# Kernel tuning notes

Hardware: AMD Instinct MI355X
Metric: run time of the kernel (lower is better)

The kernel has to match this reference:

```python
import jax, jax.numpy as jnp
import numpy as np

NH = 4
TEMP = 0.5

def _ln(x, w, b):
    mu = x.mean(-1, keepdims=True)
    var = ((x - mu) ** 2).mean(-1, keepdims=True)
    return (x - mu) / jnp.sqrt(var + 1e-5) * w + b

def _encoder(x, bias, key_pad, layers):
    # pre-LN torch TransformerEncoder, relu FFN, dropout=0
    Wqkv, bqkv, Wo, bo, ln1w, ln1b, ln2w, ln2b, W1, b1, W2, b2 = layers
    B, L, H = x.shape
    d = H // NH
    scale = 1.0 / np.sqrt(d)
    for i in range(Wqkv.shape[0]):
        y = _ln(x, ln1w[i], ln1b[i])
        qkv = y @ Wqkv[i].T + bqkv[i]
        q, k, v = jnp.split(qkv, 3, axis=-1)
        q = q.reshape(B, L, NH, d).transpose(0, 2, 1, 3)
        k = k.reshape(B, L, NH, d).transpose(0, 2, 1, 3)
        v = v.reshape(B, L, NH, d).transpose(0, 2, 1, 3)
        s = jnp.einsum('bhqd,bhkd->bhqk', q, k) * scale
        if bias is not None:
            s = s + bias
        s = s + key_pad[:, None, None, :]
        a = jax.nn.softmax(s, axis=-1)
        o = jnp.einsum('bhqk,bhkd->bhqd', a, v).transpose(0, 2, 1, 3).reshape(B, L, H)
        x = x + o @ Wo[i].T + bo[i]
        y = _ln(x, ln2w[i], ln2b[i])
        x = x + jax.nn.relu(y @ W1[i].T + b1[i]) @ W2[i].T + b2[i]
    return x

def _layer_params(key, nl, H, F, sc=0.05):
    ks = jax.random.split(key, 4)
    return (jax.random.normal(ks[0], (nl, 3 * H, H)) * sc, jnp.zeros((nl, 3 * H)),
            jax.random.normal(ks[1], (nl, H, H)) * sc, jnp.zeros((nl, H)),
            jnp.ones((nl, H)), jnp.zeros((nl, H)), jnp.ones((nl, H)), jnp.zeros((nl, H)),
            jax.random.normal(ks[2], (nl, F, H)) * sc, jnp.zeros((nl, F)),
            jax.random.normal(ks[3], (nl, H, F)) * sc, jnp.zeros((nl, H)))

def setup_inputs():
    key = jax.random.key(0)
    IN, H, ED, F = 64, 128, 16, 256
    G, NPG = 8, 512
    N = G * NPG
    m, k = 4, 16
    T = N
    S = T * m
    EPS = 24
    E_loc = S * EPS
    E = 65536
    ks = jax.random.split(key, 13)
    x = jax.random.normal(ks[0], (N, IN))
    log_probs = -jnp.abs(jax.random.normal(ks[1], (S,)))
    root = jnp.repeat(jnp.arange(T), m)
    base = (root // NPG) * NPG
    rest = base[:, None] + jax.random.randint(ks[2], (S, k - 1), 0, NPG)
    nodes_sampled = jnp.concatenate([root[:, None], rest], axis=1)
    valid = jnp.ones((S * k,), dtype=bool)
    edge_index_sampled = jax.random.randint(ks[3], (2, E_loc), 0, k)
    edge_ptr = jnp.arange(S + 1) * EPS
    ea_flat = jax.random.normal(ks[4], (E_loc, ED))
    src = jax.random.randint(ks[5], (E,), 0, N)
    dst = (src // NPG) * NPG + jax.random.randint(ks[6], (E,), 0, NPG)
    edge_index = jnp.stack([src, dst])
    edge_attr = jax.random.normal(ks[7], (E, ED))
    batch_vec = jnp.arange(N) // NPG
    ptr = jnp.arange(G + 1) * NPG
    d = dict(x=x, log_probs=log_probs, ea_flat=ea_flat, edge_attr=edge_attr,
             init_W=jax.random.normal(ks[8], (H, IN + 2)) * 0.05, init_b=jnp.zeros((H,)),
             loc_ep_W=jax.random.normal(ks[9], (NH, ED)) * 0.05, loc_ep_b=jnp.zeros((NH,)),
             glob_ep_W=jax.random.normal(ks[10], (NH, ED)) * 0.05, glob_ep_b=jnp.zeros((NH,)),
             loc_nw=jnp.ones((H,)), loc_nb=jnp.zeros((H,)),
             glob_nw=jnp.ones((H,)), glob_nb=jnp.zeros((H,)),
             nodes_sampled=nodes_sampled, edge_index_sampled=edge_index_sampled,
             edge_ptr=edge_ptr, edge_index=edge_index, batch_vec=batch_vec,
             ptr=ptr, valid=valid)
    names = ['Wqkv', 'bqkv', 'Wo', 'bo', 'ln1w', 'ln1b', 'ln2w', 'ln2b', 'W1', 'b1', 'W2', 'b2']
    for n, a in zip(names, _layer_params(ks[11], 4, H, F)):
        d['loc_' + n] = a
    for n, a in zip(names, _layer_params(ks[12], 4, H, F)):
        d['glob_' + n] = a
    return d

def reference(x, log_probs, ea_flat, edge_attr, init_W, init_b, loc_ep_W, loc_ep_b,
              glob_ep_W, glob_ep_b, loc_nw, loc_nb, glob_nw, glob_nb,
              loc_Wqkv, loc_bqkv, loc_Wo, loc_bo, loc_ln1w, loc_ln1b, loc_ln2w, loc_ln2b,
              loc_W1, loc_b1, loc_W2, loc_b2,
              glob_Wqkv, glob_bqkv, glob_Wo, glob_bo, glob_ln1w, glob_ln1b, glob_ln2w, glob_ln2b,
              glob_W1, glob_b1, glob_W2, glob_b2,
              nodes_sampled, edge_index_sampled, edge_ptr, edge_index, batch_vec, ptr, valid):
    S, k = nodes_sampled.shape
    N = x.shape[0]
    T = N
    m = S // T
    G = ptr.shape[0] - 1
    max_N = N // G  # equal-size graphs
    H = init_W.shape[0]
    # ---- phase 1: flatten subgraphs + init features ----
    x_flat = x[nodes_sampled.reshape(-1)]                         # [S*k, IN]
    root_global = jnp.repeat(jnp.arange(T), m)                    # [S]
    root_local = jnp.argmax(nodes_sampled == root_global[:, None], axis=1)
    root_mask = jnp.zeros((S * k,), x.dtype).at[jnp.arange(S) * k + root_local].set(1.0)
    lp = jnp.where(jnp.isfinite(log_probs), log_probs, 0.0)
    lp_flat = jnp.repeat(lp, k)[:, None] * valid[:, None].astype(x.dtype)
    h = jnp.concatenate([x_flat, lp_flat, root_mask[:, None]], axis=1) @ init_W.T + init_b
    # ---- local edge bias (scatter-add) ----
    E_loc = ea_flat.shape[0]
    sub = jnp.searchsorted(edge_ptr, jnp.arange(E_loc), side='right') - 1
    eap = ea_flat @ loc_ep_W.T + loc_ep_b                         # [E_loc, NH]
    lbias = jnp.zeros((S, k, k, NH), x.dtype).at[sub, edge_index_sampled[0], edge_index_sampled[1]].add(eap).transpose(0, 3, 1, 2)
    v2 = valid.reshape(S, k)
    key_pad_l = jnp.where(v2, 0.0, -1e9).astype(x.dtype)
    loc_layers = (loc_Wqkv, loc_bqkv, loc_Wo, loc_bo, loc_ln1w, loc_ln1b, loc_ln2w, loc_ln2b, loc_W1, loc_b1, loc_W2, loc_b2)
    out = _encoder(h.reshape(S, k, H), lbias, key_pad_l, loc_layers)
    out = _ln(out, loc_nw, loc_nb)
    vf = v2.astype(x.dtype)[..., None]
    sub_embs = (out * vf).sum(1) / jnp.maximum(vf.sum(1), 1.0)    # [S, H]
    # ---- weighted-mean aggregation over m samples per target node ----
    w = jax.nn.softmax(log_probs.reshape(T, m) / TEMP, axis=1)
    node_embs = jnp.einsum('tm,tmh->th', w, sub_embs.reshape(T, m, H))
    # ---- global phase: to_dense_batch + edge-bias transformer ----
    pos = jnp.arange(N) - ptr[batch_vec]
    dense = jnp.zeros((G, max_N, H), x.dtype).at[batch_vec, pos].set(node_embs)
    vmask = jnp.zeros((G, max_N), bool).at[batch_vec, pos].set(True)
    g = batch_vec[edge_index[0]]
    sl = edge_index[0] - ptr[g]
    dl = edge_index[1] - ptr[g]
    eag = edge_attr @ glob_ep_W.T + glob_ep_b
    gbias = jnp.zeros((G, max_N, max_N, NH), x.dtype).at[g, sl, dl].add(eag).transpose(0, 3, 1, 2)
    key_pad_g = jnp.where(vmask, 0.0, -1e9).astype(x.dtype)
    glob_layers = (glob_Wqkv, glob_bqkv, glob_Wo, glob_bo, glob_ln1w, glob_ln1b, glob_ln2w, glob_ln2b, glob_W1, glob_b1, glob_W2, glob_b2)
    gout = _encoder(dense, gbias, key_pad_g, glob_layers)
    gout = _ln(gout, glob_nw, glob_nb)
    return (gout * vmask[..., None].astype(x.dtype)).sum(1)      # [G, H]
```

## Files before the change

### kernel.cpp

```cpp
#include <hip/hip_runtime.h>
#include <math.h>

#define IN_F      64
#define H_DIM     128
#define NH_       4
#define DH_       32
#define FF_DIM    256
#define KSUB      16
#define S_SEQ     16384
#define E_LOC     393216
#define G_NUM     8
#define NPG_      512
#define N_NODES   4096
#define E_GLOB    65536
#define NLAYERS   4
#define SCALE_ATT 0.17677669529663687f

#define WQKV_SZ   (3*H_DIM*H_DIM)
#define WO_SZ     (H_DIM*H_DIM)
#define W1_SZ     (FF_DIM*H_DIM)
#define W2_SZ     (H_DIM*FF_DIM)

#define ATT(sg)   (4352 + (sg) * 2560)
#define PS_OFF    9472
// ... 350 lines not shown
            for (int sg = 0; sg < 2; ++sg)
                #pragma unroll
                for (int kt = 0; kt < 4; ++kt)
                    ao[sg][kt] = *(const bf16x8*)(stg + sg * 2176 + r * 136 + kt * 32 + q * 8);
            const unsigned short* wr0 = wo_l + (size_t)r * H_DIM + q * 8;
            bf16x8 co[4], no[4];
            #pragma unroll
            for (int kt = 0; kt < 4; ++kt) co[kt] = *(const bf16x8*)(wr0 + kt * 32);
            for (int nt = 0; nt < 8; ++nt) {
                if (nt < 7) {
                    const unsigned short* wn = wr0 + (size_t)(nt + 1) * 2048;
                    #pragma unroll
                    for (int kt = 0; kt < 4; ++kt) no[kt] = *(const bf16x8*)(wn + kt * 32);
                }
                f32x4 aA = {0.f,0.f,0.f,0.f}, aB = {0.f,0.f,0.f,0.f};
                PRIO_HI();
                #pragma unroll
                for (int kt = 0; kt < 4; ++kt) {
                    aA = mfma16(ao[0][kt], co[kt], aA);
                    aB = mfma16(ao[1][kt], co[kt], aB);
                }
                PRIO_LO();
                float bov = bo[l * H_DIM + nt * 16 + r];
                #pragma unroll
                for (int i = 0; i < 4; ++i) {
                    X[0][nt][i] += aA[i] + bov;
                    X[1][nt][i] += aB[i] + bov;
                }
                #pragma unroll
                for (int kt = 0; kt < 4; ++kt) co[kt] = no[kt];
            }
        }

        ln_to_row(X[0], ln2w + l * H_DIM, ln2b + l * H_DIM, stg, r, q);
        ln_to_row(X[1], ln2w + l * H_DIM, ln2b + l * H_DIM, stg + 2176, r, q);

        {
            bf16x8 a2[2][4];
            #pragma unroll
            for (int sg = 0; sg < 2; ++sg)
                #pragma unroll
                for (int kt = 0; kt < 4; ++kt)
                    a2[sg][kt] = *(const bf16x8*)(stg + sg * 2176 + r * 136 + kt * 32 + q * 8);
            const unsigned short* wr0 = w1_l + (size_t)r * H_DIM + q * 8;
            bf16x8 c1b[4], n1b[4];
            #pragma unroll
            for (int kt = 0; kt < 4; ++kt) c1b[kt] = *(const bf16x8*)(wr0 + kt * 32);
            for (int nt = 0; nt < 16; ++nt) {
                if (nt < 15) {
                    const unsigned short* wn = wr0 + (size_t)(nt + 1) * 2048;
                    #pragma unroll
                    for (int kt = 0; kt < 4; ++kt) n1b[kt] = *(const bf16x8*)(wn + kt * 32);
                }
                float b1v = b1[l * FF_DIM + nt * 16 + r];
                #pragma unroll
                for (int sg = 0; sg < 2; ++sg) {
                    f32x4 acc = {0.f,0.f,0.f,0.f};
                    PRIO_HI();
                    #pragma unroll
                    for (int kt = 0; kt < 4; ++kt) acc = mfma16(a2[sg][kt], c1b[kt], acc);
                    PRIO_LO();
                    float f0 = fmaxf(acc[0] + b1v, 0.f), f1 = fmaxf(acc[1] + b1v, 0.f);
                    float f2 = fmaxf(acc[2] + b1v, 0.f), f3 = fmaxf(acc[3] + b1v, 0.f);
                    unsigned flo = cvt_pk(f0, f1), fhi = cvt_pk(f2, f3);
                    stg[sg * 4224 + (q * 4 + 0) * 264 + nt * 16 + r] = (unsigned short)flo;
                    stg[sg * 4224 + (q * 4 + 1) * 264 + nt * 16 + r] = (unsigned short)(flo >> 16);
                    stg[sg * 4224 + (q * 4 + 2) * 264 + nt * 16 + r] = (unsigned short)fhi;
                    stg[sg * 4224 + (q * 4 + 3) * 264 + nt * 16 + r] = (unsigned short)(fhi >> 16);
                }
                #pragma unroll
                for (int kt = 0; kt < 4; ++kt) c1b[kt] = n1b[kt];
            }
            for (int kp = 0; kp < 2; ++kp) {
                bf16x8 a1[2][4];
                #pragma unroll
                for (int sg = 0; sg < 2; ++sg)
                    #pragma unroll
                    for (int kt = 0; kt < 4; ++kt)
                        a1[sg][kt] = *(const bf16x8*)(stg + sg * 4224 + r * 264 + kp * 128 + kt * 32 + q * 8);
                const unsigned short* wr2 = w2_l + (size_t)r * FF_DIM + kp * 128 + q * 8;
                bf16x8 c2b[4], n2b[4];
                #pragma unroll
                for (int kt = 0; kt < 4; ++kt) c2b[kt] = *(const bf16x8*)(wr2 + kt * 32);
                for (int nt = 0; nt < 8; ++nt) {
                    if (nt < 7) {
                        const unsigned short* wn = wr2 + (size_t)(nt + 1) * 4096;
                        #pragma unroll
                        for (int kt = 0; kt < 4; ++kt) n2b[kt] = *(const bf16x8*)(wn + kt * 32);
                    }
                    f32x4 aA = {0.f,0.f,0.f,0.f}, aB = {0.f,0.f,0.f,0.f};
                    PRIO_HI();
                    #pragma unroll
                    for (int kt = 0; kt < 4; ++kt) {
                        aA = mfma16(a1[0][kt], c2b[kt], aA);
                        aB = mfma16(a1[1][kt], c2b[kt], aB);
                    }
                    PRIO_LO();
                    float b2v = (kp == 0) ? b2[l * H_DIM + nt * 16 + r] : 0.f;
                    #pragma unroll
                    for (int i = 0; i < 4; ++i) {
                        X[0][nt][i] += aA[i] + b2v;
                        X[1][nt][i] += aB[i] + b2v;
                    }
                    #pragma unroll
                    for (int kt = 0; kt < 4; ++kt) c2b[kt] = n2b[kt];
                }
            }
        }
    }

    ln_mean_out(X[0], fnw, fnb, sub_embs + (size_t)s0 * H_DIM, r, q);
    ln_mean_out(X[1], fnw, fnb, sub_embs + (size_t)(s0 + 1) * H_DIM, r, q);
}

__global__ __launch_bounds__(256) void agg_ln_k(const float* __restrict__ sub,
    const float* __restrict__ lp, const int* __restrict__ bvec,
    const int* __restrict__ ptrg, const float* __restrict__ w,
    const float* __restrict__ b, float* __restrict__ xg,
    unsigned short* __restrict__ yout)
{
    int t = blockIdx.x * 16 + (threadIdx.x >> 4);
    int ln = threadIdx.x & 15;
    float l0 = lp[t * 4 + 0] * 2.f, l1 = lp[t * 4 + 1] * 2.f;
    float l2 = lp[t * 4 + 2] * 2.f, l3 = lp[t * 4 + 3] * 2.f;
    float mx = fmaxf(fmaxf(l0, l1), fmaxf(l2, l3));
    float e0 = __expf(l0 - mx), e1 = __expf(l1 - mx);
    float e2 = __expf(l2 - mx), e3 = __expf(l3 - mx);
    float inv = 1.f / (e0 + e1 + e2 + e3);
    e0 *= inv; e1 *= inv; e2 *= inv; e3 *= inv;
    int g = bvec[t];
    int row = g * NPG_ + (t - ptrg[g]);
    const float* sp = sub + (size_t)t * 4 * H_DIM;
    float v[8], s1 = 0.f, s2 = 0.f;
    #pragma unroll
    for (int k = 0; k < 8; ++k) {
        int i = ln + k * 16;
        float val = e0 * sp[i] + e1 * sp[H_DIM + i] + e2 * sp[2 * H_DIM + i]
                  + e3 * sp[3 * H_DIM + i];
        xg[(size_t)row * H_DIM + i] = val;
        v[k] = val; s1 += val; s2 += val * val;
    }
    for (int m2 = 8; m2 >= 1; m2 >>= 1) {
        s1 += __shfl_xor(s1, m2, 16);
        s2 += __shfl_xor(s2, m2, 16);
    }
    float mu = s1 * (1.f / H_DIM), var = s2 * (1.f / H_DIM) - mu * mu;
    float rs = rsqrtf(fmaxf(var, 0.f) + 1e-5f);
    #pragma unroll
    for (int k = 0; k < 8; ++k) {
        int i = ln + k * 16;
        yout[(size_t)row * H_DIM + i] = f2bf((v[k] - mu) * rs * w[i] + b[i]);
    }
}

__global__ __launch_bounds__(256) void zero_k(float4* __restrict__ p)
{
    p[(size_t)blockIdx.x * 256 + threadIdx.x] = make_float4(0.f, 0.f, 0.f, 0.f);
}

__global__ __launch_bounds__(256) void gbias_scatter_k(
    const float* __restrict__ edge_attr, const int* __restrict__ eidx,
    const int* __restrict__ bvec, const int* __restrict__ ptrg,
    const float* __restrict__ epW, const float* __restrict__ epb,
    float* __restrict__ gbias)
{
    int e = blockIdx.x * 256 + threadIdx.x;
    int src = eidx[e], dst = eidx[E_GLOB + e];
    int g = bvec[src];
    int sl = src - ptrg[g], dl = dst - ptrg[g];
    const float* ea = edge_attr + (size_t)e * 16;
    #pragma unroll
    for (int h = 0; h < NH_; ++h) {
        float v = epb[h];
        #pragma unroll
        for (int t = 0; t < 16; ++t) v += ea[t] * epW[h * 16 + t];
        atomicAdd(&gbias[(((size_t)g * NH_ + h) * NPG_ + sl) * NPG_ + dl], v);
    }
}

__global__ __launch_bounds__(64) void attn_fused_k(
    const unsigned short* __restrict__ qkv,
    const unsigned short* __restrict__ vt,
    const float* __restrict__ gbias,
    unsigned short* __restrict__ attg)
{
    __shared__ unsigned short pbuf[16 * 522];
    const int lane = threadIdx.x & 63;
    const int r = lane & 15, q = lane >> 4;
    const int qt = blockIdx.x, z = blockIdx.y;
    const int g = z >> 2, h = z & 3;
    const int qrow0 = qt * 16;

    bf16x8 fq = *(const bf16x8*)(qkv + (size_t)(g * NPG_ + qrow0 + r) * 384
                                 + h * DH_ + q * 8);
    const float* gb = gbias + (size_t)z * NPG_ * NPG_ + (size_t)qrow0 * NPG_;
    const unsigned short* kbase = qkv + (size_t)g * NPG_ * 384 + H_DIM + h * DH_ + q * 8;

    float mx[4] = {-1e30f, -1e30f, -1e30f, -1e30f};
    for (int kt = 0; kt < 32; ++kt) {
        bf16x8 bk = *(const bf16x8*)(kbase + (size_t)(kt * 16 + r) * 384);
        f32x4 sc = mfma16(fq, bk, (f32x4){0.f,0.f,0.f,0.f});
        #pragma unroll
        for (int i = 0; i < 4; ++i)
            mx[i] = fmaxf(mx[i],
                sc[i] * SCALE_ATT + gb[(size_t)(q * 4 + i) * NPG_ + kt * 16 + r]);
    }
    #pragma unroll
    for (int i = 0; i < 4; ++i) {
        mx[i] = fmaxf(mx[i], __shfl_xor(mx[i], 1, 16));
        mx[i] = fmaxf(mx[i], __shfl_xor(mx[i], 2, 16));
        mx[i] = fmaxf(mx[i], __shfl_xor(mx[i], 4, 16));
        mx[i] = fmaxf(mx[i], __shfl_xor(mx[i], 8, 16));
    }

    float sm[4] = {0.f, 0.f, 0.f, 0.f};
    for (int kt = 0; kt < 32; ++kt) {
        bf16x8 bk = *(const bf16x8*)(kbase + (size_t)(kt * 16 + r) * 384);
        f32x4 sc = mfma16(fq, bk, (f32x4){0.f,0.f,0.f,0.f});
        float e0 = __expf(sc[0] * SCALE_ATT + gb[(size_t)(q * 4 + 0) * NPG_ + kt * 16 + r] - mx[0]);
        float e1 = __expf(sc[1] * SCALE_ATT + gb[(size_t)(q * 4 + 1) * NPG_ + kt * 16 + r] - mx[1]);
        float e2 = __expf(sc[2] * SCALE_ATT + gb[(size_t)(q * 4 + 2) * NPG_ + kt * 16 + r] - mx[2]);
        float e3 = __expf(sc[3] * SCALE_ATT + gb[(size_t)(q * 4 + 3) * NPG_ + kt * 16 + r] - mx[3]);
        sm[0] += e0; sm[1] += e1; sm[2] += e2; sm[3] += e3;
        unsigned lo = cvt_pk(e0, e1), hi = cvt_pk(e2, e3);
        pbuf[(q * 4 + 0) * 522 + kt * 16 + r] = (unsigned short)lo;
        pbuf[(q * 4 + 1) * 522 + kt * 16 + r] = (unsigned short)(lo >> 16);
        pbuf[(q * 4 + 2) * 522 + kt * 16 + r] = (unsigned short)hi;
        pbuf[(q * 4 + 3) * 522 + kt * 16 + r] = (unsigned short)(hi >> 16);
    }
    float inv[4];
    #pragma unroll
    for (int i = 0; i < 4; ++i) {
        float s = sm[i];
        s += __shfl_xor(s, 1, 16); s += __shfl_xor(s, 2, 16);
        s += __shfl_xor(s, 4, 16); s += __shfl_xor(s, 8, 16);
        inv[i] = 1.f / s;
    }

    f32x4 oa = {0.f,0.f,0.f,0.f}, ob = {0.f,0.f,0.f,0.f};
    const unsigned short* v0p = vt + (size_t)(z * 32 + r) * NPG_;
    const unsigned short* v1p = vt + (size_t)(z * 32 + 16 + r) * NPG_;
    for (int kc = 0; kc < 16; ++kc) {
        bf16x8 ap  = *(const bf16x8*)(pbuf + r * 522 + kc * 32 + q * 8);
        bf16x8 bv0 = *(const bf16x8*)(v0p + kc * 32 + q * 8);
        bf16x8 bv1 = *(const bf16x8*)(v1p + kc * 32 + q * 8);
        oa = mfma16(ap, bv0, oa);
        ob = mfma16(ap, bv1, ob);
    }
    #pragma unroll
    for (int i = 0; i < 4; ++i) {
        size_t row = (size_t)(g * NPG_ + qrow0 + q * 4 + i) * H_DIM + h * DH_;
        attg[row + r]      = f2bf(oa[i] * inv[i]);
        attg[row + 16 + r] = f2bf(ob[i] * inv[i]);
    }
}

__global__ __launch_bounds__(256) void gemm_mfma_k(
    const unsigned short* __restrict__ A, const unsigned short* __restrict__ B,
    void* __restrict__ Cv, const float* __restrict__ bias, const float* __restrict__ D,
    unsigned short* __restrict__ vtout,
    int M, int N, int K, int lda, int ldb, int ldc, int ldd,
    long sAg, long sAh, long sBg, long sBh, long sCg, long sCh, long sDg, long sDh,
    float alpha, int op)
{
    const int z = blockIdx.z, zg = z >> 2, zh = z & 3;
    A += zg * sAg + zh * sAh;
    B += zg * sBg + zh * sBh;
    const int lane = threadIdx.x & 63, wave = threadIdx.x >> 6;
    const int r = lane & 15, q = lane >> 4;
    const int m0 = blockIdx.y * 64 + wave * 16;
    const int n0 = blockIdx.x * 64;
    const int ntiles = min(4, (N - n0) >> 4);
    const int KT = K >> 5;
    const unsigned short* ap = A + (size_t)(m0 + r) * lda + q * 8;
    for (int nt = 0; nt < ntiles; ++nt) {
        const int col = n0 + nt * 16 + r;
        const unsigned short* bp = B + (size_t)col * ldb + q * 8;
        f32x4 acc = {0.f, 0.f, 0.f, 0.f};
        for (int kc = 0; kc < KT; ++kc) {
            bf16x8 av = *(const bf16x8*)(ap + kc * 32);
            bf16x8 bv = *(const bf16x8*)(bp + kc * 32);
            acc = mfma16(av, bv, acc);
        }
        float bv2 = bias ? bias[col] : 0.f;
        #pragma unroll
        for (int i = 0; i < 4; ++i) {
            const int row = m0 + q * 4 + i;
            if (op == 0) {
                ((unsigned short*)Cv)[zg * sCg + zh * sCh + (size_t)row * ldc + col] =
                    f2bf(acc[i] + bv2);
            } else {
                unsigned short hv = f2bf(acc[i] + bv2);
                ((unsigned short*)Cv)[(size_t)row * ldc + col] = hv;
                if (col >= 256) {
                    int h = (col - 256) >> 5, d = (col - 256) & 31;
                    int g = row >> 9, tok = row & 511;
                    vtout[(((size_t)(g * 4 + h)) * 32 + d) * 512 + tok] = hv;
                }
            }
        }
    }
}

__global__ __launch_bounds__(64) void layer_tail_k(
    const unsigned short* __restrict__ attg,
    const unsigned short* __restrict__ wo,
    const unsigned short* __restrict__ w1,
    const unsigned short* __restrict__ w2,
    const float* __restrict__ bo, const float* __restrict__ b1,
    const float* __restrict__ b2,
    float* __restrict__ xg,
    const float* __restrict__ ln2w, const float* __restrict__ ln2b,
    const float* __restrict__ nw, const float* __restrict__ nb,
    void* __restrict__ yout, int mode)
{
    __shared__ unsigned short stg2[16 * 264];
    const int lane = threadIdx.x & 63;
    const int r = lane & 15, q = lane >> 4;
    const int m0 = blockIdx.x * 16;

    float X[8][4];
    #pragma unroll
    for (int nt = 0; nt < 8; ++nt)
        #pragma unroll
        for (int i = 0; i < 4; ++i)
            X[nt][i] = xg[(size_t)(m0 + q * 4 + i) * H_DIM + nt * 16 + r];

    {
        bf16x8 ao[4];
        #pragma unroll
        for (int kt = 0; kt < 4; ++kt)
            ao[kt] = *(const bf16x8*)(attg + (size_t)(m0 + r) * H_DIM + kt * 32 + q * 8);
        const unsigned short* wr0 = wo + (size_t)r * H_DIM + q * 8;
        bf16x8 co[4], no[4];
        #pragma unroll
        for (int kt = 0; kt < 4; ++kt) co[kt] = *(const bf16x8*)(wr0 + kt * 32);
        for (int nt = 0; nt < 8; ++nt) {
            if (nt < 7) {
                const unsigned short* wn = wr0 + (size_t)(nt + 1) * 2048;
                #pragma unroll
                for (int kt = 0; kt < 4; ++kt) no[kt] = *(const bf16x8*)(wn + kt * 32);
            }
            f32x4 acc = {0.f,0.f,0.f,0.f};
            PRIO_HI();
            #pragma unroll
            for (int kt = 0; kt < 4; ++kt) acc = mfma16(ao[kt], co[kt], acc);
            PRIO_LO();
            float bov = bo[nt * 16 + r];
            #pragma unroll
            for (int i = 0; i < 4; ++i) X[nt][i] += acc[i] + bov;
            #pragma unroll
            for (int kt = 0; kt < 4; ++kt) co[kt] = no[kt];
        }
    }

    ln_to_row(X, ln2w, ln2b, stg2, r, q);

    {
        bf16x8 a2[4];
        #pragma unroll
        for (int kt = 0; kt < 4; ++kt)
            a2[kt] = *(const bf16x8*)(stg2 + r * 136 + kt * 32 + q * 8);
        const unsigned short* wr0 = w1 + (size_t)r * H_DIM + q * 8;
        bf16x8 c1b[4], n1b[4];
        #pragma unroll
        for (int kt = 0; kt < 4; ++kt) c1b[kt] = *(const bf16x8*)(wr0 + kt * 32);
        for (int nt = 0; nt < 16; ++nt) {
            if (nt < 15) {
                const unsigned short* wn = wr0 + (size_t)(nt + 1) * 2048;
                #pragma unroll
                for (int kt = 0; kt < 4; ++kt) n1b[kt] = *(const bf16x8*)(wn + kt * 32);
            }
            float b1v = b1[nt * 16 + r];
            f32x4 acc = {0.f,0.f,0.f,0.f};
            PRIO_HI();
            #pragma unroll
            for (int kt = 0; kt < 4; ++kt) acc = mfma16(a2[kt], c1b[kt], acc);
            PRIO_LO();
            float f0 = fmaxf(acc[0] + b1v, 0.f), f1 = fmaxf(acc[1] + b1v, 0.f);
            float f2 = fmaxf(acc[2] + b1v, 0.f), f3 = fmaxf(acc[3] + b1v, 0.f);
            unsigned flo = cvt_pk(f0, f1), fhi = cvt_pk(f2, f3);
            stg2[(q * 4 + 0) * 264 + nt * 16 + r] = (unsigned short)flo;
            stg2[(q * 4 + 1) * 264 + nt * 16 + r] = (unsigned short)(flo >> 16);
            stg2[(q * 4 + 2) * 264 + nt * 16 + r] = (unsigned short)fhi;
            stg2[(q * 4 + 3) * 264 + nt * 16 + r] = (unsigned short)(fhi >> 16);
            #pragma unroll
            for (int kt = 0; kt < 4; ++kt) c1b[kt] = n1b[kt];
        }
        for (int kp = 0; kp < 2; ++kp) {
            bf16x8 a1[4];
            #pragma unroll
            for (int kt = 0; kt < 4; ++kt)
                a1[kt] = *(const bf16x8*)(stg2 + r * 264 + kp * 128 + kt * 32 + q * 8);
            const unsigned short* wr2 = w2 + (size_t)r * FF_DIM + kp * 128 + q * 8;
            bf16x8 c2b[4], n2b[4];
            #pragma unroll
            for (int kt = 0; kt < 4; ++kt) c2b[kt] = *(const bf16x8*)(wr2 + kt * 32);
            for (int nt = 0; nt < 8; ++nt) {
                if (nt < 7) {
                    const unsigned short* wn = wr2 + (size_t)(nt + 1) * 4096;
                    #pragma unroll
                    for (int kt = 0; kt < 4; ++kt) n2b[kt] = *(const bf16x8*)(wn + kt * 32);
                }
                f32x4 acc = {0.f,0.f,0.f,0.f};
                PRIO_HI();
                #pragma unroll
                for (int kt = 0; kt < 4; ++kt) acc = mfma16(a1[kt], c2b[kt], acc);
                PRIO_LO();
                float b2v = (kp == 0) ? b2[nt * 16 + r] : 0.f;
                #pragma unroll
                for (int i = 0; i < 4; ++i) X[nt][i] += acc[i] + b2v;
                #pragma unroll
                for (int kt = 0; kt < 4; ++kt) c2b[kt] = n2b[kt];
            }
        }
    }

    #pragma unroll
    for (int nt = 0; nt < 8; ++nt)
        #pragma unroll
        for (int i = 0; i < 4; ++i)
            xg[(size_t)(m0 + q * 4 + i) * H_DIM + nt * 16 + r] = X[nt][i];

    float s1[4] = {0,0,0,0}, s2[4] = {0,0,0,0};
    #pragma unroll
    for (int nt = 0; nt < 8; ++nt)
        #pragma unroll
        for (int i = 0; i < 4; ++i) { float x = X[nt][i]; s1[i] += x; s2[i] += x * x; }
    #pragma unroll
    for (int i = 0; i < 4; ++i) {
        float a = s1[i], c = s2[i];
        a += __shfl_xor(a, 1, 16); a += __shfl_xor(a, 2, 16);
        a += __shfl_xor(a, 4, 16); a += __shfl_xor(a, 8, 16);
        c += __shfl_xor(c, 1, 16); c += __shfl_xor(c, 2, 16);
        c += __shfl_xor(c, 4, 16); c += __shfl_xor(c, 8, 16);
        float mu = a * (1.f / H_DIM);
        float var = c * (1.f / H_DIM) - mu * mu;
        s1[i] = mu; s2[i] = rsqrtf(fmaxf(var, 0.f) + 1e-5f);
    }
    #pragma unroll
    for (int nt = 0; nt < 8; ++nt) {
        const int col = nt * 16 + r;
        float wv = nw[col], bv = nb[col];
        #pragma unroll
        for (int i = 0; i < 4; ++i) {
            const int row = m0 + q * 4 + i;
            float ln = (X[nt][i] - s1[i]) * s2[i] * wv + bv;
            if (mode == 0) ((unsigned short*)yout)[(size_t)row * H_DIM + col] = f2bf(ln);
            else           ((float*)yout)[(size_t)row * H_DIM + col] = ln;
        }
    }
}

__global__ __launch_bounds__(1024) void reduce_out_k(const float* __restrict__ yg,
                                                     float* __restrict__ out)
{
    __shared__ float part[8][128];
    int g = blockIdx.x;
    int i = threadIdx.x & 127, c = threadIdx.x >> 7;
    float s = 0.f;
    const float* base = yg + ((size_t)(g * NPG_ + c * 64)) * H_DIM + i;
    for (int t = 0; t < 64; ++t) s += base[(size_t)t * H_DIM];
    part[c][i] = s;
    __syncthreads();
    if (threadIdx.x < 128) {
        float acc = 0.f;
        #pragma unroll
        for (int c2 = 0; c2 < 8; ++c2) acc += part[c2][threadIdx.x];
        out[g * H_DIM + threadIdx.x] = acc;
    }
}

extern "C" void kernel_launch(void* const* d_in, const int* in_sizes, int n_in,
                              void* d_out, int out_size, void* d_ws, size_t ws_size,
                              hipStream_t stream)
{
    const float* x         = (const float*)d_in[0];
    const float* lp        = (const float*)d_in[1];
    const float* ea_flat   = (const float*)d_in[2];
    const float* edge_attr = (const float*)d_in[3];
    const float* init_W    = (const float*)d_in[4];
    const float* init_b    = (const float*)d_in[5];
    const float* lepW      = (const float*)d_in[6];
    const float* lepb      = (const float*)d_in[7];
    const float* gepW      = (const float*)d_in[8];
    const float* gepb      = (const float*)d_in[9];
    const float* lnw       = (const float*)d_in[10];
    const float* lnb       = (const float*)d_in[11];
    const float* gnw       = (const float*)d_in[12];
    const float* gnb       = (const float*)d_in[13];
    const int*   nodes     = (const int*)d_in[14];
    const int*   eis       = (const int*)d_in[15];
    const int*   eptr      = (const int*)d_in[16];  (void)eptr;
    const int*   eidx      = (const int*)d_in[17];
    const int*   bvec      = (const int*)d_in[18];
    const int*   ptrg      = (const int*)d_in[19];
    const float* lWqkv = (const float*)d_in[21];
    const float* lbqkv = (const float*)d_in[22];
    const float* lWo   = (const float*)d_in[23];
    const float* lbo   = (const float*)d_in[24];
    const float* lln1w = (const float*)d_in[25];
    const float* lln1b = (const float*)d_in[26];
    const float* lln2w = (const float*)d_in[27];
    const float* lln2b = (const float*)d_in[28];
    const float* lW1   = (const float*)d_in[29];
    const float* lb1   = (const float*)d_in[30];
    const float* lW2   = (const float*)d_in[31];
    const float* lb2   = (const float*)d_in[32];
    const float* gWqkv = (const float*)d_in[33];
    const float* gbqkv = (const float*)d_in[34];
    const float* gWo   = (const float*)d_in[35];
    const float* gbo   = (const float*)d_in[36];
    const float* gln1w = (const float*)d_in[37];
    const float* gln1b = (const float*)d_in[38];
    const float* gln2w = (const float*)d_in[39];
    const float* gln2b = (const float*)d_in[40];
    const float* gW1   = (const float*)d_in[41];
    const float* gb1   = (const float*)d_in[42];
    const float* gW2   = (const float*)d_in[43];
    const float* gb2   = (const float*)d_in[44];

    float* out = (float*)d_out;
    float* ws  = (float*)d_ws;
    float* gbias   = ws;
    float* scores  = ws + 8388608;
    float* subembs = scores;
    float* xg      = ws + 16777216;
    unsigned short* qkvg_b = (unsigned short*)(ws + 17301504);
    unsigned short* yg_b   = (unsigned short*)(ws + 18087936);
    unsigned short* attg_b = (unsigned short*)(ws + 18350080);
    unsigned short* ffg_b  = (unsigned short*)(ws + 18612224);
    unsigned short* vt_b   = (unsigned short*)(ws + 19136512);
    unsigned short* gw     = (unsigned short*)(ws + 19398656);
    (void)ffg_b;

    unsigned short* wb   = (unsigned short*)gbias;
    unsigned short* wq_b = wb;
    unsigned short* wo_b = wb + 196608;
    unsigned short* w1_b = wb + 262144;
    unsigned short* w2_b = wb + 393216;
    unsigned short* x_b  = wb + 524288;
    unsigned short* wi_b = wb + 786432;
    unsigned short* gwq_b = gw;
    unsigned short* gwo_b = gw + 196608;
    unsigned short* gw1_b = gw + 262144;
    unsigned short* gw2_b = gw + 393216;

    hipLaunchKernelGGL(conv_all_k, dim3(5152), dim3(256), 0, stream,
        lWqkv, lWo, lW1, lW2, x, gWqkv, gWo, gW1, gW2, init_W,
        wq_b, wo_b, w1_b, w2_b, x_b, gwq_b, gwo_b, gw1_b, gw2_b, wi_b);

    hipLaunchKernelGGL(local_encoder_k, dim3(S_SEQ / 2), dim3(64), 0, stream,
        x_b, lp, ea_flat, init_W, init_b, wi_b, lepW, lepb, nodes, eis,
        wq_b, wo_b, w1_b, w2_b,
        lbqkv, lbo, lln1w, lln1b, lln2w, lln2b, lb1, lb2,
        lnw, lnb, subembs);

    hipLaunchKernelGGL(agg_ln_k, dim3(N_NODES / 16), dim3(256), 0, stream,
        subembs, lp, bvec, ptrg, gln1w, gln1b, xg, yg_b);

    hipLaunchKernelGGL(zero_k, dim3(8192), dim3(256), 0, stream, (float4*)gbias);
    hipLaunchKernelGGL(gbias_scatter_k, dim3(E_GLOB / 256), dim3(256), 0, stream,
        edge_attr, eidx, bvec, ptrg, gepW, gepb, gbias);

    for (int l = 0; l < NLAYERS; ++l) {
        {
            dim3 grid((384 + 63) / 64, 4096 / 64, 1);
            hipLaunchKernelGGL(gemm_mfma_k, grid, dim3(256), 0, stream,
                yg_b, gwq_b + (size_t)l * WQKV_SZ, qkvg_b,
                gbqkv + l * 384, nullptr, vt_b, 4096, 384, 128, 128, 128, 384, 0,
                0, 0, 0, 0, 0, 0, 0, 0, 1.f, 4);
        }
        hipLaunchKernelGGL(attn_fused_k, dim3(NPG_ / 16, 32), dim3(64), 0, stream,
            qkvg_b, vt_b, gbias, attg_b);
        const float* nw = (l < 3) ? (gln1w + (l + 1) * H_DIM) : gnw;
        const float* nb = (l < 3) ? (gln1b + (l + 1) * H_DIM) : gnb;
        void* yo = (l < 3) ? (void*)yg_b : (void*)scores;
        hipLaunchKernelGGL(layer_tail_k, dim3(N_NODES / 16), dim3(64), 0, stream,
            attg_b, gwo_b + (size_t)l * WO_SZ, gw1_b + (size_t)l * W1_SZ,
            gw2_b + (size_t)l * W2_SZ,
            gbo + l * H_DIM, gb1 + l * FF_DIM, gb2 + l * H_DIM,
            xg, gln2w + l * H_DIM, gln2b + l * H_DIM,
            nw, nb, yo, (l < 3) ? 0 : 1);
    }

    hipLaunchKernelGGL(reduce_out_k, dim3(G_NUM), dim3(1024), 0, stream, scores, out);
}
```

Before: 1.358 ms.

## Split global layer tail across four waves per 16-row block

The global-encoder layer tail kernel (Wo projection, LN2, FFN, final LN) now uses four wavefronts per 16-row tile instead of one. Each wave owns a slice of output columns, and the LayerNorm statistics are combined across waves through shared memory with block barriers. The goal is more parallelism and latency hiding for a kernel that previously ran 256 single-wave blocks serially over all column tiles. The cost is extra __syncthreads and LDS reductions, and the register double-buffered weight prefetch is dropped.

```diff
diff --git a/kernel.cpp b/kernel.cpp
--- a/kernel.cpp
+++ b/kernel.cpp
@@ -676,7 +676,7 @@
     }
 }
 
-__global__ __launch_bounds__(64) void layer_tail_k(
+__global__ __launch_bounds__(256) void layer_tail4_k(
     const unsigned short* __restrict__ attg,
     const unsigned short* __restrict__ wo,
     const unsigned short* __restrict__ w1,
@@ -688,138 +688,197 @@
     const float* __restrict__ nw, const float* __restrict__ nb,
     void* __restrict__ yout, int mode)
 {
-    __shared__ unsigned short stg2[16 * 264];
-    const int lane = threadIdx.x & 63;
+    __shared__ unsigned short yb[16 * 136];
+    __shared__ unsigned short ffb[16 * 264];
+    __shared__ float red[4][2][16];
+    const int lane = threadIdx.x & 63, w = threadIdx.x >> 6;
     const int r = lane & 15, q = lane >> 4;
     const int m0 = blockIdx.x * 16;
 
-    float X[8][4];
-    #pragma unroll
-    for (int nt = 0; nt < 8; ++nt)
+    float X[2][4];
+    #pragma unroll
+    for (int j = 0; j < 2; ++j) {
+        const int nt = 2 * w + j;
         #pragma unroll
         for (int i = 0; i < 4; ++i)
-            X[nt][i] = xg[(size_t)(m0 + q * 4 + i) * H_DIM + nt * 16 + r];
+            X[j][i] = xg[(size_t)(m0 + q * 4 + i) * H_DIM + nt * 16 + r];
+    }
 
     {
         bf16x8 ao[4];
         #pragma unroll
         for (int kt = 0; kt < 4; ++kt)
             ao[kt] = *(const bf16x8*)(attg + (size_t)(m0 + r) * H_DIM + kt * 32 + q * 8);
-        const unsigned short* wr0 = wo + (size_t)r * H_DIM + q * 8;
-        bf16x8 co[4], no[4];
-        #pragma unroll
-        for (int kt = 0; kt < 4; ++kt) co[kt] = *(const bf16x8*)(wr0 + kt * 32);
-        for (int nt = 0; nt < 8; ++nt) {
-            if (nt < 7) {
-                const unsigned short* wn = wr0 + (size_t)(nt + 1) * 2048;
-                #pragma unroll
-                for (int kt = 0; kt < 4; ++kt) no[kt] = *(const bf16x8*)(wn + kt * 32);
-            }
+        #pragma unroll
+        for (int j = 0; j < 2; ++j) {
+            const int nt = 2 * w + j;
+            const unsigned short* wr = wo + (size_t)(nt * 16 + r) * H_DIM + q * 8;
+            bf16x8 c0 = *(const bf16x8*)(wr);
+            bf16x8 c1 = *(const bf16x8*)(wr + 32);
+            bf16x8 c2 = *(const bf16x8*)(wr + 64);
+            bf16x8 c3 = *(const bf16x8*)(wr + 96);
             f32x4 acc = {0.f,0.f,0.f,0.f};
             PRIO_HI();
-            #pragma unroll
-            for (int kt = 0; kt < 4; ++kt) acc = mfma16(ao[kt], co[kt], acc);
+            acc = mfma16(ao[0], c0, acc); acc = mfma16(ao[1], c1, acc);
+            acc = mfma16(ao[2], c2, acc); acc = mfma16(ao[3], c3, acc);
             PRIO_LO();
             float bov = bo[nt * 16 + r];
             #pragma unroll
-            for (int i = 0; i < 4; ++i) X[nt][i] += acc[i] + bov;
-            #pragma unroll
-            for (int kt = 0; kt < 4; ++kt) co[kt] = no[kt];
-        }
-    }
-
-    ln_to_row(X, ln2w, ln2b, stg2, r, q);
+            for (int i = 0; i < 4; ++i) X[j][i] += acc[i] + bov;
+        }
+    }
+
+    float mu[4], rs[4];
+    {
+        float s1[4], s2[4];
+        #pragma unroll
+        for (int i = 0; i < 4; ++i) {
+            float a = X[0][i] + X[1][i];
+            float c = X[0][i] * X[0][i] + X[1][i] * X[1][i];
+            a += __shfl_xor(a, 1, 16); a += __shfl_xor(a, 2, 16);
+            a += __shfl_xor(a, 4, 16); a += __shfl_xor(a, 8, 16);
+            c += __shfl_xor(c, 1, 16); c += __shfl_xor(c, 2, 16);
+            c += __shfl_xor(c, 4, 16); c += __shfl_xor(c, 8, 16);
+            s1[i] = a; s2[i] = c;
+        }
+        if (r == 0) {
+            #pragma unroll
+            for (int i = 0; i < 4; ++i) {
+                red[w][0][q * 4 + i] = s1[i];
+                red[w][1][q * 4 + i] = s2[i];
+            }
+        }
+        __syncthreads();
+        #pragma unroll
+        for (int i = 0; i < 4; ++i) {
+            float a = red[0][0][q*4+i] + red[1][0][q*4+i] + red[2][0][q*4+i] + red[3][0][q*4+i];
+            float c = red[0][1][q*4+i] + red[1][1][q*4+i] + red[2][1][q*4+i] + red[3][1][q*4+i];
+            float m = a * (1.f / H_DIM);
+            float var = c * (1.f / H_DIM) - m * m;
+            mu[i] = m; rs[i] = rsqrtf(fmaxf(var, 0.f) + 1e-5f);
+        }
+    }
+
+    #pragma unroll
+    for (int j = 0; j < 2; ++j) {
+        const int nt = 2 * w + j;
+        const int col = nt * 16 + r;
+        float wv = ln2w[col], bv = ln2b[col];
+        float v0 = (X[0 + 0][0] - mu[0]) * rs[0] * 0.f;  (void)v0;
+        float y0 = (X[j][0] - mu[0]) * rs[0] * wv + bv;
+        float y1 = (X[j][1] - mu[1]) * rs[1] * wv + bv;
+        float y2 = (X[j][2] - mu[2]) * rs[2] * wv + bv;
+        float y3 = (X[j][3] - mu[3]) * rs[3] * wv + bv;
+        unsigned lo = cvt_pk(y0, y1), hi = cvt_pk(y2, y3);
+        yb[(q * 4 + 0) * 136 + col] = (unsigned short)lo;
+        yb[(q * 4 + 1) * 136 + col] = (unsigned short)(lo >> 16);
+        yb[(q * 4 + 2) * 136 + col] = (unsigned short)hi;
+        yb[(q * 4 + 3) * 136 + col] = (unsigned short)(hi >> 16);
+    }
+    __syncthreads();
 
     {
         bf16x8 a2[4];
         #pragma unroll
         for (int kt = 0; kt < 4; ++kt)
-            a2[kt] = *(const bf16x8*)(stg2 + r * 136 + kt * 32 + q * 8);
-        const unsigned short* wr0 = w1 + (size_t)r * H_DIM + q * 8;
-        bf16x8 c1b[4], n1b[4];
-        #pragma unroll
-        for (int kt = 0; kt < 4; ++kt) c1b[kt] = *(const bf16x8*)(wr0 + kt * 32);
-        for (int nt = 0; nt < 16; ++nt) {
-            if (nt < 15) {
-                const unsigned short* wn = wr0 + (size_t)(nt + 1) * 2048;
-                #pragma unroll
-                for (int kt = 0; kt < 4; ++kt) n1b[kt] = *(const bf16x8*)(wn + kt * 32);
-            }
-            float b1v = b1[nt * 16 + r];
+            a2[kt] = *(const bf16x8*)(yb + r * 136 + kt * 32 + q * 8);
+        #pragma unroll
+        for (int j2 = 0; j2 < 4; ++j2) {
+            const int nt = 4 * w + j2;
+            const unsigned short* wr = w1 + (size_t)(nt * 16 + r) * H_DIM + q * 8;
+            bf16x8 c0 = *(const bf16x8*)(wr);
+            bf16x8 c1 = *(const bf16x8*)(wr + 32);
+            bf16x8 c2 = *(const bf16x8*)(wr + 64);
+            bf16x8 c3 = *(const bf16x8*)(wr + 96);
             f32x4 acc = {0.f,0.f,0.f,0.f};
             PRIO_HI();
-            #pragma unroll
-            for (int kt = 0; kt < 4; ++kt) acc = mfma16(a2[kt], c1b[kt], acc);
+            acc = mfma16(a2[0], c0, acc); acc = mfma16(a2[1], c1, acc);
+            acc = mfma16(a2[2], c2, acc); acc = mfma16(a2[3], c3, acc);
             PRIO_LO();
+            float b1v = b1[nt * 16 + r];
             float f0 = fmaxf(acc[0] + b1v, 0.f), f1 = fmaxf(acc[1] + b1v, 0.f);
             float f2 = fmaxf(acc[2] + b1v, 0.f), f3 = fmaxf(acc[3] + b1v, 0.f);
             unsigned flo = cvt_pk(f0, f1), fhi = cvt_pk(f2, f3);
-            stg2[(q * 4 + 0) * 264 + nt * 16 + r] = (unsigned short)flo;
-            stg2[(q * 4 + 1) * 264 + nt * 16 + r] = (unsigned short)(flo >> 16);
-            stg2[(q * 4 + 2) * 264 + nt * 16 + r] = (unsigned short)fhi;
-            stg2[(q * 4 + 3) * 264 + nt * 16 + r] = (unsigned short)(fhi >> 16);
-            #pragma unroll
-            for (int kt = 0; kt < 4; ++kt) c1b[kt] = n1b[kt];
-        }
-        for (int kp = 0; kp < 2; ++kp) {
-            bf16x8 a1[4];
-            #pragma unroll
-            for (int kt = 0; kt < 4; ++kt)
-                a1[kt] = *(const bf16x8*)(stg2 + r * 264 + kp * 128 + kt * 32 + q * 8);
-            const unsigned short* wr2 = w2 + (size_t)r * FF_DIM + kp * 128 + q * 8;
-            bf16x8 c2b[4], n2b[4];
-            #pragma unroll
-            for (int kt = 0; kt < 4; ++kt) c2b[kt] = *(const bf16x8*)(wr2 + kt * 32);
-            for (int nt = 0; nt < 8; ++nt) {
-                if (nt < 7) {
-                    const unsigned short* wn = wr2 + (size_t)(nt + 1) * 4096;
-                    #pragma unroll
-                    for (int kt = 0; kt < 4; ++kt) n2b[kt] = *(const bf16x8*)(wn + kt * 32);
-                }
-                f32x4 acc = {0.f,0.f,0.f,0.f};
-                PRIO_HI();
-                #pragma unroll
-                for (int kt = 0; kt < 4; ++kt) acc = mfma16(a1[kt], c2b[kt], acc);
-                PRIO_LO();
-                float b2v = (kp == 0) ? b2[nt * 16 + r] : 0.f;
-                #pragma unroll
-                for (int i = 0; i < 4; ++i) X[nt][i] += acc[i] + b2v;
-                #pragma unroll
-                for (int kt = 0; kt < 4; ++kt) c2b[kt] = n2b[kt];
+            ffb[(q * 4 + 0) * 264 + nt * 16 + r] = (unsigned short)flo;
+            ffb[(q * 4 + 1) * 264 + nt * 16 + r] = (unsigned short)(flo >> 16);
+            ffb[(q * 4 + 2) * 264 + nt * 16 + r] = (unsigned short)fhi;
+            ffb[(q * 4 + 3) * 264 + nt * 16 + r] = (unsigned short)(fhi >> 16);
+        }
+    }
+    __syncthreads();
+
+    for (int kp = 0; kp < 2; ++kp) {
+        bf16x8 a1[4];
+        #pragma unroll
+        for (int kt = 0; kt < 4; ++kt)
+            a1[kt] = *(const bf16x8*)(ffb + r * 264 + kp * 128 + kt * 32 + q * 8);
+        #pragma unroll
+        for (int j = 0; j < 2; ++j) {
+            const int nt = 2 * w + j;
+            const unsigned short* wr = w2 + (size_t)(nt * 16 + r) * FF_DIM + kp * 128 + q * 8;
+            bf16x8 c0 = *(const bf16x8*)(wr);
+            bf16x8 c1 = *(const bf16x8*)(wr + 32);
+            bf16x8 c2 = *(const bf16x8*)(wr + 64);
+            bf16x8 c3 = *(const bf16x8*)(wr + 96);
+            f32x4 acc = {0.f,0.f,0.f,0.f};
+            PRIO_HI();
+            acc = mfma16(a1[0], c0, acc); acc = mfma16(a1[1], c1, acc);
+            acc = mfma16(a1[2], c2, acc); acc = mfma16(a1[3], c3, acc);
+            PRIO_LO();
+            float b2v = (kp == 0) ? b2[nt * 16 + r] : 0.f;
+            #pragma unroll
+            for (int i = 0; i < 4; ++i) X[j][i] += acc[i] + b2v;
+        }
+    }
+
+    #pragma unroll
+    for (int j = 0; j < 2; ++j) {
+        const int nt = 2 * w + j;
+        #pragma unroll
+        for (int i = 0; i < 4; ++i)
+            xg[(size_t)(m0 + q * 4 + i) * H_DIM + nt * 16 + r] = X[j][i];
+    }
+
+    {
+        float s1[4], s2[4];
+        #pragma unroll
+        for (int i = 0; i < 4; ++i) {
+            float a = X[0][i] + X[1][i];
+            float c = X[0][i] * X[0][i] + X[1][i] * X[1][i];
+            a += __shfl_xor(a, 1, 16); a += __shfl_xor(a, 2, 16);
+            a += __shfl_xor(a, 4, 16); a += __shfl_xor(a, 8, 16);
+            c += __shfl_xor(c, 1, 16); c += __shfl_xor(c, 2, 16);
+            c += __shfl_xor(c, 4, 16); c += __shfl_xor(c, 8, 16);
+            s1[i] = a; s2[i] = c;
+        }
+        __syncthreads();
+        if (r == 0) {
+            #pragma unroll
+            for (int i = 0; i < 4; ++i) {
+                red[w][0][q * 4 + i] = s1[i];
+                red[w][1][q * 4 + i] = s2[i];
             }
         }
-    }
-
-    #pragma unroll
-    for (int nt = 0; nt < 8; ++nt)
-        #pragma unroll
-        for (int i = 0; i < 4; ++i)
-            xg[(size_t)(m0 + q * 4 + i) * H_DIM + nt * 16 + r] = X[nt][i];
-
-    float s1[4] = {0,0,0,0}, s2[4] = {0,0,0,0};
-    #pragma unroll
-    for (int nt = 0; nt < 8; ++nt)
-        #pragma unroll
-        for (int i = 0; i < 4; ++i) { float x = X[nt][i]; s1[i] += x; s2[i] += x * x; }
-    #pragma unroll
-    for (int i = 0; i < 4; ++i) {
-        float a = s1[i], c = s2[i];
-        a += __shfl_xor(a, 1, 16); a += __shfl_xor(a, 2, 16);
-        a += __shfl_xor(a, 4, 16); a += __shfl_xor(a, 8, 16);
-        c += __shfl_xor(c, 1, 16); c += __shfl_xor(c, 2, 16);
-        c += __shfl_xor(c, 4, 16); c += __shfl_xor(c, 8, 16);
-        float mu = a * (1.f / H_DIM);
-        float var = c * (1.f / H_DIM) - mu * mu;
-        s1[i] = mu; s2[i] = rsqrtf(fmaxf(var, 0.f) + 1e-5f);
-    }
-    #pragma unroll
-    for (int nt = 0; nt < 8; ++nt) {
+        __syncthreads();
+        #pragma unroll
+        for (int i = 0; i < 4; ++i) {
+            float a = red[0][0][q*4+i] + red[1][0][q*4+i] + red[2][0][q*4+i] + red[3][0][q*4+i];
+            float c = red[0][1][q*4+i] + red[1][1][q*4+i] + red[2][1][q*4+i] + red[3][1][q*4+i];
+            float m = a * (1.f / H_DIM);
+            float var = c * (1.f / H_DIM) - m * m;
+            mu[i] = m; rs[i] = rsqrtf(fmaxf(var, 0.f) + 1e-5f);
+        }
+    }
+
+    #pragma unroll
+    for (int j = 0; j < 2; ++j) {
+        const int nt = 2 * w + j;
         const int col = nt * 16 + r;
         float wv = nw[col], bv = nb[col];
         #pragma unroll
         for (int i = 0; i < 4; ++i) {
             const int row = m0 + q * 4 + i;
-            float ln = (X[nt][i] - s1[i]) * s2[i] * wv + bv;
+            float ln = (X[j][i] - mu[i]) * rs[i] * wv + bv;
             if (mode == 0) ((unsigned short*)yout)[(size_t)row * H_DIM + col] = f2bf(ln);
             else           ((float*)yout)[(size_t)row * H_DIM + col] = ln;
         }
@@ -950,7 +1009,7 @@
         const float* nw = (l < 3) ? (gln1w + (l + 1) * H_DIM) : gnw;
         const float* nb = (l < 3) ? (gln1b + (l + 1) * H_DIM) : gnb;
         void* yo = (l < 3) ? (void*)yg_b : (void*)scores;
-        hipLaunchKernelGGL(layer_tail_k, dim3(N_NODES / 16), dim3(64), 0, stream,
+        hipLaunchKernelGGL(layer_tail4_k, dim3(N_NODES / 16), dim3(256), 0, stream,
             attg_b, gwo_b + (size_t)l * WO_SZ, gw1_b + (size_t)l * W1_SZ,
             gw2_b + (size_t)l * W2_SZ,
             gbo + l * H_DIM, gb1 + l * FF_DIM, gb2 + l * H_DIM,
```

Measured after the change: 1.322 ms. 2.7% less time.
